# Kernel tuning notes

Measured on AMD Instinct MI355X. Metric: run time of the kernel, lower is better.

## Reference

```python
import jax, jax.numpy as jnp
import numpy as np
from jax.ops import segment_sum, segment_max

N = 50000   # nodes
E = 800000  # directed edges
H, C = 4, 64  # GAT heads, per-head channels (hidden_dim//4)
HID = 256
EPS = 1e-5


def setup_inputs() -> dict:
    key = jax.random.key(0)
    ks = jax.random.split(key, 24)
    g = lambda k, shape, fan: jax.random.normal(k, shape, jnp.float32) * (1.0 / np.sqrt(fan))
    inp = {
        'x': jax.random.normal(ks[0], (N, 3), jnp.float32),
        'edge_index': jax.random.randint(ks[1], (2, E), 0, N, jnp.int32),
        # GCNConv 1: 3 -> 64
        'W1': g(ks[2], (3, 64), 3), 'b1': jnp.zeros((64,), jnp.float32),
        # GCNConv 2: 64 -> 128
        'W2': g(ks[3], (64, 128), 64), 'b2': jnp.zeros((128,), jnp.float32),
        # GATConv: 128 -> 4 heads x 64
        'Wg': g(ks[4], (128, H * C), 128),
        'a_src': g(ks[5], (H, C), C), 'a_dst': g(ks[6], (H, C), C),
        'bg': jnp.zeros((H * C,), jnp.float32),
        # LayerNorms
        'ln1_g': jnp.ones((64,), jnp.float32), 'ln1_b': jnp.zeros((64,), jnp.float32),
        'ln2_g': jnp.ones((128,), jnp.float32), 'ln2_b': jnp.zeros((128,), jnp.float32),
        'ln3_g': jnp.ones((HID,), jnp.float32), 'ln3_b': jnp.zeros((HID,), jnp.float32),
        # GlobalAttention gate: Linear(256,256) ReLU Linear(256,1)
        'Wgt1': g(ks[7], (HID, HID), HID), 'bgt1': jnp.zeros((HID,), jnp.float32),
        'Wgt2': g(ks[8], (HID, 1), HID), 'bgt2': jnp.zeros((1,), jnp.float32),
        # output mlp: Linear(256,256) ReLU
        'Wm': g(ks[9], (HID, HID), HID), 'bm': jnp.zeros((HID,), jnp.float32),
    }
    return inp


def _ln(x, g, b):
    mu = x.mean(-1, keepdims=True)
    var = ((x - mu) ** 2).mean(-1, keepdims=True)
    return g * (x - mu) * jax.lax.rsqrt(var + EPS) + b


def reference(x, edge_index, W1, b1, W2, b2, Wg, a_src, a_dst, bg,
              ln1_g, ln1_b, ln2_g, ln2_b, ln3_g, ln3_b,
              Wgt1, bgt1, Wgt2, bgt2, Wm, bm):
    n = x.shape[0]
    loop = jnp.arange(n, dtype=edge_index.dtype)
    src = jnp.concatenate([edge_index[0], loop])  # self-loops added (PyG default)
    dst = jnp.concatenate([edge_index[1], loop])

    # symmetric GCN normalization (deg counts self-loop)
    deg = segment_sum(jnp.ones_like(src, jnp.float32), dst, num_segments=n)
    dinv = jax.lax.rsqrt(jnp.maximum(deg, 1.0))
    norm = (dinv[src] * dinv[dst])[:, None]  # [E+N,1]

    def gcn(h, W, b):
        h = h @ W
        return segment_sum(norm * h[src], dst, num_segments=n) + b

    x1 = _ln(jax.nn.relu(gcn(x, W1, b1)), ln1_g, ln1_b)
    x2 = _ln(jax.nn.relu(gcn(x1, W2, b2)), ln2_g, ln2_b)

    # GATConv: per-head scores, segment-softmax over destination
    h = (x2 @ Wg).reshape(n, H, C)
    s_src = (h * a_src).sum(-1)  # [N,H]
    s_dst = (h * a_dst).sum(-1)
    e = jax.nn.leaky_relu(s_src[src] + s_dst[dst], 0.2)  # [E+N,H]
    m = segment_max(e, dst, num_segments=n)
    ex = jnp.exp(e - m[dst])
    den = segment_sum(ex, dst, num_segments=n)
    alpha = ex / (den[dst] + 1e-16)  # [E+N,H]
    agg = segment_sum(alpha[:, :, None] * h[src], dst, num_segments=n)  # [N,H,C]
    x3 = _ln(agg.reshape(n, H * C) + bg, ln3_g, ln3_b)

    # GlobalAttention pooling (batch=None -> single graph)
    gate = jax.nn.relu(x3 @ Wgt1 + bgt1) @ Wgt2 + bgt2  # [N,1]
    w = jax.nn.softmax(gate, axis=0)
    pooled = (w * x3).sum(0, keepdims=True)  # [1,256]
    out = jax.nn.relu(pooled @ Wm + bm)  # [1,256]
    return out, x3
```

## Files before the change

### kernel.cpp

```cpp
#include <hip/hip_runtime.h>
#include <math.h>

#define NNODES 50000
#define NEDGES 800000

__device__ __forceinline__ float wave_sum(float v) {
#pragma unroll
  for (int o = 32; o > 0; o >>= 1) v += __shfl_xor(v, o, 64);
  return v;
}
__device__ __forceinline__ float wave_max(float v) {
#pragma unroll
  for (int o = 32; o > 0; o >>= 1) v = fmaxf(v, __shfl_xor(v, o, 64));
  return v;
}
template <int NW>
__device__ __forceinline__ float block_sum(float v, float* red) {
  v = wave_sum(v);
  __syncthreads();
  if ((threadIdx.x & 63) == 0) red[threadIdx.x >> 6] = v;
  __syncthreads();
  float s = 0.f;
#pragma unroll
  for (int i = 0; i < NW; i++) s += red[i];
  return s;
}

__device__ __forceinline__ float leaky02(float x) { return x > 0.f ? x : 0.2f * x; }

__device__ __forceinline__ void atomicMaxFloat(float* addr, float val) {
  if (val >= 0.f)
    atomicMax((int*)addr, __float_as_int(val));
  else
    atomicMin((unsigned int*)addr, __float_as_uint(val));
}

__global__ void k_init(int* __restrict__ deg, float* __restrict__ scal,
                       float* __restrict__ pooled) {
  int i = blockIdx.x * blockDim.x + threadIdx.x;
  if (i < NNODES) deg[i] = 0;
  if (i < 256) pooled[i] = 0.f;
  if (i == 0) { scal[0] = -3.0e38f; scal[1] = 0.f; }
}

__global__ void k_deg(const int* __restrict__ dst, int* __restrict__ deg) {
  int e = blockIdx.x * blockDim.x + threadIdx.x;
  if (e < NEDGES) atomicAdd(&deg[dst[e]], 1);
}

__global__ __launch_bounds__(1024) void k_scan(const int* __restrict__ deg,
                                               int* __restrict__ offs,
                                               int* __restrict__ cursor,
                                               float* __restrict__ dinv) {
  __shared__ int lds[1024];
  const int t = threadIdx.x;
  const int chunk = (NNODES + 1023) / 1024;
  int lo = t * chunk, hi = min(lo + chunk, NNODES);
  int s = 0;
  for (int i = lo; i < hi; i++) s += deg[i];
  lds[t] = s;
  __syncthreads();
  for (int off = 1; off < 1024; off <<= 1) {
    int v = (t >= off) ? lds[t - off] : 0;
    __syncthreads();
    lds[t] += v;
    __syncthreads();
  }
  int base = (t > 0) ? lds[t - 1] : 0;
  for (int i = lo; i < hi; i++) {
    int d = deg[i];
    offs[i] = base;
    cursor[i] = base;
    dinv[i] = rsqrtf((float)(d + 1));
    base += d;
  }
  if (t == 1023) offs[NNODES] = lds[1023];
}

__global__ void k_fill(const int* __restrict__ src, const int* __restrict__ dst,
                       int* __restrict__ cursor, int* __restrict__ csr) {
  int e = blockIdx.x * blockDim.x + threadIdx.x;
  if (e >= NEDGES) return;
  int d = dst[e];
  int p = atomicAdd(&cursor[d], 1);
  csr[p] = src[e];
}

__global__ void k_agg3(const float* __restrict__ x, const float* __restrict__ dinv,
                       const int* __restrict__ offs, const int* __restrict__ csr,
                       float* __restrict__ agg0) {
  int n = blockIdx.x * blockDim.x + threadIdx.x;
  if (n >= NNODES) return;
  float di = dinv[n];
  float a0 = di * x[n * 3], a1 = di * x[n * 3 + 1], a2 = di * x[n * 3 + 2];
  int lo = offs[n], hi = offs[n + 1];
  int p = lo;
  int snext = (p < hi) ? csr[p] : 0;
  while (p < hi) {
    int s = snext; p++; if (p < hi) snext = csr[p];
    float w = dinv[s];
    a0 = fmaf(w, x[s * 3], a0);
    a1 = fmaf(w, x[s * 3 + 1], a1);
    a2 = fmaf(w, x[s * 3 + 2], a2);
  }
  agg0[n * 3] = di * a0; agg0[n * 3 + 1] = di * a1; agg0[n * 3 + 2] = di * a2;
}

template <int VEC, int NG>
__global__ __launch_bounds__(64 * NG) void k_agg(const float* __restrict__ h,
                                                 const float* __restrict__ dinv,
                                                 const int* __restrict__ offs,
                                                 const int* __restrict__ csr,
                                                 float* __restrict__ out) {
  __shared__ float lacc[NG][64][VEC + 1];
  const int n = blockIdx.x;
  const int lane = threadIdx.x & 63, g = threadIdx.x >> 6;
  const float di = dinv[n];
  float acc[VEC];
#pragma unroll
  for (int v = 0; v < VEC; v++) acc[v] = 0.f;
  if (g == 0) {
    const float* r = h + (size_t)n * (64 * VEC) + lane * VEC;
#pragma unroll
    for (int v = 0; v < VEC; v++) acc[v] = di * r[v];
  }
  const int lo = offs[n], hi = offs[n + 1];
  int p = lo + g;
  int snext = (p < hi) ? csr[p] : 0;
  while (p < hi) {
    int s = snext; p += NG; if (p < hi) snext = csr[p];
    float w = dinv[s];
    const float* r = h + (size_t)s * (64 * VEC) + lane * VEC;
#pragma unroll
    for (int v = 0; v < VEC; v++) acc[v] = fmaf(w, r[v], acc[v]);
  }
#pragma unroll
  for (int v = 0; v < VEC; v++) lacc[g][lane][v] = acc[v];
  __syncthreads();
  if (g == 0) {
#pragma unroll
    for (int G = 1; G < NG; G++)
#pragma unroll
      for (int v = 0; v < VEC; v++) acc[v] += lacc[G][lane][v];
    float* o = out + (size_t)n * (64 * VEC) + lane * VEC;
#pragma unroll
    for (int v = 0; v < VEC; v++) o[v] = di * acc[v];
  }
}

template <int K, int M, int NT, bool RELU>
__global__ void k_mlp(const float* __restrict__ X, const float* __restrict__ W,
                      const float* __restrict__ b, const float* __restrict__ gam,
                      const float* __restrict__ bet, float* __restrict__ Y) {
  constexpr int NW = M / 64;
  __shared__ float xs[NT * K];
  __shared__ float red[NW];
  const int n0 = blockIdx.x * NT;
  const int j = threadIdx.x;
  const float4* Xt = (const float4*)(X + (size_t)n0 * K);
  for (int i = j; i < NT * K / 4; i += M) ((float4*)xs)[i] = Xt[i];
  __syncthreads();
  float acc[NT];
  float bj = b[j];
#pragma unroll
  for (int r = 0; r < NT; r++) acc[r] = bj;
  for (int k = 0; k < K; k++) {
    float wk = W[k * M + j];
#pragma unroll
    for (int r = 0; r < NT; r++) acc[r] = fmaf(xs[r * K + k], wk, acc[r]);
  }
  float gj = gam[j], btj = bet[j];
  for (int r = 0; r < NT; r++) {
    float a = RELU ? fmaxf(acc[r], 0.f) : acc[r];
    float mu = block_sum<NW>(a, red) * (1.f / M);
    float d = a - mu;
    float var = block_sum<NW>(d * d, red) * (1.f / M);
    Y[(size_t)(n0 + r) * M + j] = fmaf(gj * d, rsqrtf(var + 1e-5f), btj);
  }
}

__global__ void k_uvec(const float* __restrict__ Wg, const float* __restrict__ a_src,
                       const float* __restrict__ a_dst, float* __restrict__ u) {
  const int t = threadIdx.x;
  const int hh = t >> 7, k = t & 127;
  float us = 0.f, ud = 0.f;
  for (int c = 0; c < 64; c++) {
    float w = Wg[k * 256 + hh * 64 + c];
    us = fmaf(w, a_src[hh * 64 + c], us);
    ud = fmaf(w, a_dst[hh * 64 + c], ud);
  }
  u[t] = us;
  u[512 + t] = ud;
}

__global__ __launch_bounds__(256) void k_scores(const float* __restrict__ x2,
                                                const float* __restrict__ u,
                                                float* __restrict__ ssrc,
                                                float* __restrict__ sdst) {
  __shared__ float us[1024];
  const int t = threadIdx.x;
  for (int i = t; i < 1024; i += 256) us[i] = u[i];
  __syncthreads();
  const int n = blockIdx.x * 4 + (t >> 6);
  const int lane = t & 63;
  if (n >= NNODES) return;
  float2 xv = *(const float2*)(x2 + (size_t)n * 128 + lane * 2);
  float d[8];
#pragma unroll
  for (int h = 0; h < 4; h++) {
    d[h] = xv.x * us[h * 128 + lane * 2] + xv.y * us[h * 128 + lane * 2 + 1];
    d[4 + h] = xv.x * us[512 + h * 128 + lane * 2] + xv.y * us[512 + h * 128 + lane * 2 + 1];
  }
#pragma unroll
  for (int o = 32; o > 0; o >>= 1) {
#pragma unroll
    for (int i = 0; i < 8; i++) d[i] += __shfl_xor(d[i], o, 64);
  }
  if (lane == 0) {
    *(float4*)(ssrc + (size_t)n * 4) = make_float4(d[0], d[1], d[2], d[3]);
    *(float4*)(sdst + (size_t)n * 4) = make_float4(d[4], d[5], d[6], d[7]);
  }
}

__global__ __launch_bounds__(256) void k_gatagg(const float* __restrict__ x2,
                                                const float* __restrict__ ssrc,
                                                const float* __restrict__ sdst,
                                                const int* __restrict__ offs,
                                                const int* __restrict__ csr,
                                                float* __restrict__ aggx, int nbase) {
  __shared__ float lm[4][4];
  __shared__ float lden[4][4];
  __shared__ float lacc[4][64][9];
  const int n = nbase + blockIdx.x;
  const int t = threadIdx.x;
  const int lane = t & 63, g = t >> 6;
  const float4 sd = *(const float4*)(sdst + (size_t)n * 4);
  const int lo = offs[n], hi = offs[n + 1];
  float m0 = -3.4e38f, m1 = -3.4e38f, m2 = -3.4e38f, m3 = -3.4e38f;
  float e0x = 0.f, e0y = 0.f, e0z = 0.f, e0w = 0.f;
  if (g == 0) {
    float4 s0 = *(const float4*)(ssrc + (size_t)n * 4);
    e0x = leaky02(s0.x + sd.x); e0y = leaky02(s0.y + sd.y);
    e0z = leaky02(s0.z + sd.z); e0w = leaky02(s0.w + sd.w);
    m0 = e0x; m1 = e0y; m2 = e0z; m3 = e0w;
  }
  for (int p = lo + g; p < hi; p += 4) {
    int s = csr[p];
    float4 ss = *(const float4*)(ssrc + (size_t)s * 4);
    m0 = fmaxf(m0, leaky02(ss.x + sd.x));
    m1 = fmaxf(m1, leaky02(ss.y + sd.y));
    m2 = fmaxf(m2, leaky02(ss.z + sd.z));
    m3 = fmaxf(m3, leaky02(ss.w + sd.w));
  }
  if (lane == 0) { lm[g][0] = m0; lm[g][1] = m1; lm[g][2] = m2; lm[g][3] = m3; }
  __syncthreads();
  const float M0 = fmaxf(fmaxf(lm[0][0], lm[1][0]), fmaxf(lm[2][0], lm[3][0]));
  const float M1 = fmaxf(fmaxf(lm[0][1], lm[1][1]), fmaxf(lm[2][1], lm[3][1]));
  const float M2 = fmaxf(fmaxf(lm[0][2], lm[1][2]), fmaxf(lm[2][2], lm[3][2]));
  const float M3 = fmaxf(fmaxf(lm[0][3], lm[1][3]), fmaxf(lm[2][3], lm[3][3]));
  float den0 = 0.f, den1 = 0.f, den2 = 0.f, den3 = 0.f;
  float a0x = 0.f, a0y = 0.f, a1x = 0.f, a1y = 0.f;
  float a2x = 0.f, a2y = 0.f, a3x = 0.f, a3y = 0.f;
  if (g == 0) {
    float2 xv = *(const float2*)(x2 + (size_t)n * 128 + lane * 2);
    float w;
    w = __expf(e0x - M0); den0 = w; a0x = w * xv.x; a0y = w * xv.y;
    w = __expf(e0y - M1); den1 = w; a1x = w * xv.x; a1y = w * xv.y;
    w = __expf(e0z - M2); den2 = w; a2x = w * xv.x; a2y = w * xv.y;
    w = __expf(e0w - M3); den3 = w; a3x = w * xv.x; a3y = w * xv.y;
  }
  int p = lo + g;
  int snext = (p < hi) ? csr[p] : 0;
  while (p < hi) {
    int s = snext; p += 4; if (p < hi) snext = csr[p];
    float4 ss = *(const float4*)(ssrc + (size_t)s * 4);
    float2 xv = *(const float2*)(x2 + (size_t)s * 128 + lane * 2);
    float w0 = __expf(leaky02(ss.x + sd.x) - M0);
    float w1 = __expf(leaky02(ss.y + sd.y) - M1);
    float w2 = __expf(leaky02(ss.z + sd.z) - M2);
    float w3 = __expf(leaky02(ss.w + sd.w) - M3);
    den0 += w0; den1 += w1; den2 += w2; den3 += w3;
    a0x = fmaf(w0, xv.x, a0x); a0y = fmaf(w0, xv.y, a0y);
    a1x = fmaf(w1, xv.x, a1x); a1y = fmaf(w1, xv.y, a1y);
    a2x = fmaf(w2, xv.x, a2x); a2y = fmaf(w2, xv.y, a2y);
    a3x = fmaf(w3, xv.x, a3x); a3y = fmaf(w3, xv.y, a3y);
  }
  if (lane == 0) { lden[g][0] = den0; lden[g][1] = den1; lden[g][2] = den2; lden[g][3] = den3; }
  lacc[g][lane][0] = a0x; lacc[g][lane][1] = a0y;
  lacc[g][lane][2] = a1x; lacc[g][lane][3] = a1y;
  lacc[g][lane][4] = a2x; lacc[g][lane][5] = a2y;
  lacc[g][lane][6] = a3x; lacc[g][lane][7] = a3y;
  __syncthreads();
  float den = lden[0][g] + lden[1][g] + lden[2][g] + lden[3][g] + 1e-16f;
  float ax = lacc[0][lane][2 * g] + lacc[1][lane][2 * g] + lacc[2][lane][2 * g] + lacc[3][lane][2 * g];
  float ay = lacc[0][lane][2 * g + 1] + lacc[1][lane][2 * g + 1] + lacc[2][lane][2 * g + 1] + lacc[3][lane][2 * g + 1];
  float2 ov; ov.x = ax / den; ov.y = ay / den;
  *(float2*)(aggx + (size_t)blockIdx.x * 512 + g * 128 + lane * 2) = ov;
}

__global__ __launch_bounds__(256) void k_proj(const float* __restrict__ aggx,
                                              const float* __restrict__ Wg,
                                              const float* __restrict__ bg,
                                              const float* __restrict__ gam,
                                              const float* __restrict__ bet,
                                              float* __restrict__ x3, int nbase) {
  __shared__ float xs[8 * 512];
  __shared__ float red[4];
  const int r0 = blockIdx.x * 8;
  const int j = threadIdx.x;
  const int head = j >> 6;
  const float4* At = (const float4*)(aggx + (size_t)r0 * 512);
  for (int i = j; i < 1024; i += 256) ((float4*)xs)[i] = At[i];
  __syncthreads();
  float acc[8];
  float bgj = bg[j];
#pragma unroll
  for (int r = 0; r < 8; r++) acc[r] = bgj;
  for (int k = 0; k < 128; k++) {
    float wk = Wg[k * 256 + j];
#pragma unroll
    for (int r = 0; r < 8; r++) acc[r] = fmaf(xs[r * 512 + head * 128 + k], wk, acc[r]);
  }
  float gj = gam[j], btj = bet[j];
  for (int r = 0; r < 8; r++) {
    float a = acc[r];
    float mu = block_sum<4>(a, red) * (1.f / 256.f);
    float d = a - mu;
    float var = block_sum<4>(d * d, red) * (1.f / 256.f);
    x3[(size_t)(nbase + r0 + r) * 256 + j] = fmaf(gj * d, rsqrtf(var + 1e-5f), btj);
  }
}

__global__ __launch_bounds__(256) void k_gate(const float* __restrict__ x3,
                                              const float* __restrict__ Wgt1,
                                              const float* __restrict__ bgt1,
                                              const float* __restrict__ Wgt2,
                                              const float* __restrict__ bgt2,
                                              float* __restrict__ gate) {
  __shared__ float xs[16 * 256];
  __shared__ float hs[16 * 256];
  const int n0 = blockIdx.x * 16;
  const int j = threadIdx.x;
  const float4* Xt = (const float4*)(x3 + (size_t)n0 * 256);
  for (int i = j; i < 1024; i += 256) ((float4*)xs)[i] = Xt[i];
  __syncthreads();
  float acc[16];
  float b1j = bgt1[j];
#pragma unroll
  for (int r = 0; r < 16; r++) acc[r] = b1j;
  for (int k = 0; k < 256; k++) {
    float wk = Wgt1[k * 256 + j];
#pragma unroll
    for (int r = 0; r < 16; r++) acc[r] = fmaf(xs[r * 256 + k], wk, acc[r]);
  }
  float w2 = Wgt2[j];
#pragma unroll
  for (int r = 0; r < 16; r++) hs[r * 256 + j] = fmaxf(acc[r], 0.f) * w2;
  __syncthreads();
  const int wv = j >> 6, lane = j & 63;
  float b2 = bgt2[0];
#pragma unroll
  for (int rr = 0; rr < 4; rr++) {
    int r = wv * 4 + rr;
    float s = hs[r * 256 + lane] + hs[r * 256 + 64 + lane] +
              hs[r * 256 + 128 + lane] + hs[r * 256 + 192 + lane];
    s = wave_sum(s);
    if (lane == 0) gate[n0 + r] = s + b2;
  }
}

__global__ void k_gmax(const float* __restrict__ gate, float* __restrict__ scal) {
  __shared__ float red[4];
  int i = blockIdx.x * 256 + threadIdx.x;
  float v = (i < NNODES) ? gate[i] : -3.0e38f;
  v = wave_max(v);
  __syncthreads();
  if ((threadIdx.x & 63) == 0) red[threadIdx.x >> 6] = v;
  __syncthreads();
  if (threadIdx.x == 0) {
    float m = fmaxf(fmaxf(red[0], red[1]), fmaxf(red[2], red[3]));
    atomicMaxFloat(&scal[0], m);
  }
}

__global__ void k_pool(const float* __restrict__ x3, const float* __restrict__ gate,
                       const float* __restrict__ scal, float* __restrict__ pooled) {
  const int c = threadIdx.x;
  const float gmax = scal[0];
  float acc = 0.f, zl = 0.f;
  for (int node = blockIdx.x; node < NNODES; node += gridDim.x) {
    float wv = __expf(gate[node] - gmax);
    if (c == 0) zl += wv;
    acc = fmaf(wv, x3[(size_t)node * 256 + c], acc);
  }
  atomicAdd(&pooled[c], acc);
  if (c == 0) atomicAdd((float*)&scal[1], zl);
}

__global__ void k_out(const float* __restrict__ pooled, const float* __restrict__ scal,
                      const float* __restrict__ Wm, const float* __restrict__ bm,
                      float* __restrict__ out) {
  __shared__ float p[256];
  const int j = threadIdx.x;
  p[j] = pooled[j] / scal[1];
  __syncthreads();
  float acc = bm[j];
  for (int k = 0; k < 256; k++) acc = fmaf(p[k], Wm[k * 256 + j], acc);
  out[j] = fmaxf(acc, 0.f);
}

extern "C" void kernel_launch(void* const* d_in, const int* in_sizes, int n_in,
                              void* d_out, int out_size, void* d_ws, size_t ws_size,
                              hipStream_t stream) {
  const float* x     = (const float*)d_in[0];
  const int*   ei    = (const int*)d_in[1];
  const float* W1    = (const float*)d_in[2];
  const float* b1    = (const float*)d_in[3];
  const float* W2    = (const float*)d_in[4];
  const float* b2    = (const float*)d_in[5];
  const float* Wg    = (const float*)d_in[6];
  const float* a_src = (const float*)d_in[7];
  const float* a_dst = (const float*)d_in[8];
  const float* bg    = (const float*)d_in[9];
  const float* ln1g  = (const float*)d_in[10];
  const float* ln1b  = (const float*)d_in[11];
  const float* ln2g  = (const float*)d_in[12];
  const float* ln2b  = (const float*)d_in[13];
  const float* ln3g  = (const float*)d_in[14];
  const float* ln3b  = (const float*)d_in[15];
  const float* Wgt1  = (const float*)d_in[16];
  const float* bgt1  = (const float*)d_in[17];
  const float* Wgt2  = (const float*)d_in[18];
  const float* bgt2  = (const float*)d_in[19];
  const float* Wm    = (const float*)d_in[20];
  const float* bm    = (const float*)d_in[21];

  float* out = (float*)d_out;
  float* x3  = out + 256;

  const int* src = ei;
  const int* dst = ei + NEDGES;

  char* wsb = (char*)d_ws;
  size_t off = 0;
  auto carve = [&](size_t bytes) -> void* {
    void* p = wsb + off;
    off += (bytes + 255) & ~(size_t)255;
    return p;
  };
  int*   deg    = (int*)carve((size_t)NNODES * 4);
  int*   offs   = (int*)carve((size_t)(NNODES + 1) * 4);
  int*   cursor = (int*)carve((size_t)NNODES * 4);
  int*   csr    = (int*)carve((size_t)NEDGES * 4);
  float* dinv   = (float*)carve((size_t)NNODES * 4);
  float* bufA   = (float*)carve((size_t)NNODES * 256 * 4);
  float* x2     = (float*)carve((size_t)NNODES * 128 * 4);
  float* ssrc   = (float*)carve((size_t)NNODES * 4 * 4);
  float* sdst   = (float*)carve((size_t)NNODES * 4 * 4);
  float* u      = (float*)carve(1024 * 4);
  float* gate   = (float*)carve((size_t)NNODES * 4);
  float* pooled = (float*)carve(256 * 4);
  float* scal   = (float*)carve(2 * 4);

  float* x1   = bufA;
  float* agg1 = bufA + (size_t)NNODES * 64;
  float* agg0 = bufA + (size_t)NNODES * 128;
  float* aggx = bufA;

  k_init<<<(NNODES + 255) / 256, 256, 0, stream>>>(deg, scal, pooled);
  k_deg<<<NEDGES / 256, 256, 0, stream>>>(dst, deg);
  k_scan<<<1, 1024, 0, stream>>>(deg, offs, cursor, dinv);
  k_fill<<<NEDGES / 256, 256, 0, stream>>>(src, dst, cursor, csr);

  k_agg3<<<(NNODES + 255) / 256, 256, 0, stream>>>(x, dinv, offs, csr, agg0);
  k_mlp<3, 64, 16, true><<<NNODES / 16, 64, 0, stream>>>(agg0, W1, b1, ln1g, ln1b, x1);

  k_agg<1, 4><<<NNODES, 256, 0, stream>>>(x1, dinv, offs, csr, agg1);
  k_mlp<64, 128, 8, true><<<NNODES / 8, 128, 0, stream>>>(agg1, W2, b2, ln2g, ln2b, x2);

  k_uvec<<<1, 512, 0, stream>>>(Wg, a_src, a_dst, u);
  k_scores<<<(NNODES + 3) / 4, 256, 0, stream>>>(x2, u, ssrc, sdst);
  for (int c = 0; c < 2; c++) {
    int nbase = c * (NNODES / 2);
    k_gatagg<<<NNODES / 2, 256, 0, stream>>>(x2, ssrc, sdst, offs, csr, aggx, nbase);
    k_proj<<<NNODES / 2 / 8, 256, 0, stream>>>(aggx, Wg, bg, ln3g, ln3b, x3, nbase);
  }

  k_gate<<<NNODES / 16, 256, 0, stream>>>(x3, Wgt1, bgt1, Wgt2, bgt2, gate);
  k_gmax<<<(NNODES + 255) / 256, 256, 0, stream>>>(gate, scal);
  k_pool<<<256, 256, 0, stream>>>(x3, gate, scal, pooled);
  k_out<<<1, 256, 0, stream>>>(pooled, scal, Wm, bm, out);
}
```

Before: 957.2 us.

## Register-tile the GAT projection and gate GEMMs with 4x4 per-thread outputs

Rewrites k_proj and k_gate so each thread computes a 4-row by 4-column output tile using float4 loads of both the shared-memory activations and the global weights. Each weight and activation value loaded is then reused across four outputs instead of one. LayerNorm and the gate reduction become per-wave shuffles, which removes the block-wide __syncthreads reductions and the hs shared buffer. k_proj now handles 16 rows per block, pads its shared rows to stride 132, and adds bounds checks. The cost is more registers per thread and fewer blocks in flight for k_proj.

```diff
diff --git a/kernel.cpp b/kernel.cpp
--- a/kernel.cpp
+++ b/kernel.cpp
@@ -303,31 +303,73 @@
                                               const float* __restrict__ bg,
                                               const float* __restrict__ gam,
                                               const float* __restrict__ bet,
-                                              float* __restrict__ x3, int nbase) {
-  __shared__ float xs[8 * 512];
-  __shared__ float red[4];
-  const int r0 = blockIdx.x * 8;
-  const int j = threadIdx.x;
-  const int head = j >> 6;
-  const float4* At = (const float4*)(aggx + (size_t)r0 * 512);
-  for (int i = j; i < 1024; i += 256) ((float4*)xs)[i] = At[i];
-  __syncthreads();
-  float acc[8];
-  float bgj = bg[j];
-#pragma unroll
-  for (int r = 0; r < 8; r++) acc[r] = bgj;
-  for (int k = 0; k < 128; k++) {
-    float wk = Wg[k * 256 + j];
-#pragma unroll
-    for (int r = 0; r < 8; r++) acc[r] = fmaf(xs[r * 512 + head * 128 + k], wk, acc[r]);
-  }
-  float gj = gam[j], btj = bet[j];
-  for (int r = 0; r < 8; r++) {
-    float a = acc[r];
-    float mu = block_sum<4>(a, red) * (1.f / 256.f);
-    float d = a - mu;
-    float var = block_sum<4>(d * d, red) * (1.f / 256.f);
-    x3[(size_t)(nbase + r0 + r) * 256 + j] = fmaf(gj * d, rsqrtf(var + 1e-5f), btj);
+                                              float* __restrict__ x3, int nbase,
+                                              int nrows) {
+  __shared__ float xs[16][4 * 132];
+  const int r0 = blockIdx.x * 16;
+  const int t = threadIdx.x;
+  const int cq = t & 63, rq = t >> 6;
+  const int h = cq >> 4;
+  for (int idx = t; idx < 16 * 128; idx += 256) {
+    int r = idx >> 7;
+    int p = (idx & 127) << 2;
+    int hh = p >> 7, k = p & 127;
+    float4 v = (r0 + r < nrows)
+                   ? *(const float4*)(aggx + (size_t)(r0 + r) * 512 + p)
+                   : make_float4(0.f, 0.f, 0.f, 0.f);
+    *(float4*)&xs[r][hh * 132 + k] = v;
+  }
+  __syncthreads();
+  float acc[4][4];
+#pragma unroll
+  for (int i = 0; i < 4; i++)
+#pragma unroll
+    for (int j = 0; j < 4; j++) acc[i][j] = 0.f;
+  const float4* Wv = (const float4*)Wg;
+  for (int k0 = 0; k0 < 128; k0 += 4) {
+    float4 xk[4], wk[4];
+#pragma unroll
+    for (int i = 0; i < 4; i++)
+      xk[i] = *(const float4*)&xs[rq * 4 + i][h * 132 + k0];
+#pragma unroll
+    for (int kk = 0; kk < 4; kk++) wk[kk] = Wv[(size_t)(k0 + kk) * 64 + cq];
+#pragma unroll
+    for (int kk = 0; kk < 4; kk++) {
+      const float* wf = (const float*)&wk[kk];
+#pragma unroll
+      for (int i = 0; i < 4; i++) {
+        const float* xf = (const float*)&xk[i];
+        float xv = xf[kk];
+#pragma unroll
+        for (int j = 0; j < 4; j++) acc[i][j] = fmaf(xv, wf[j], acc[i][j]);
+      }
+    }
+  }
+  float4 bgv = *(const float4*)(bg + cq * 4);
+  float4 gav = *(const float4*)(gam + cq * 4);
+  float4 bev = *(const float4*)(bet + cq * 4);
+  const float* bgf = (const float*)&bgv;
+  const float* gaf = (const float*)&gav;
+  const float* bef = (const float*)&bev;
+#pragma unroll
+  for (int i = 0; i < 4; i++) {
+    float a[4], s = 0.f;
+#pragma unroll
+    for (int j = 0; j < 4; j++) { a[j] = acc[i][j] + bgf[j]; s += a[j]; }
+    float mu = wave_sum(s) * (1.f / 256.f);
+    float s2 = 0.f;
+#pragma unroll
+    for (int j = 0; j < 4; j++) { float d = a[j] - mu; s2 += d * d; }
+    float rs = rsqrtf(wave_sum(s2) * (1.f / 256.f) + 1e-5f);
+    int r = r0 + rq * 4 + i;
+    if (r < nrows) {
+      float4 ov;
+      ov.x = fmaf(gaf[0] * (a[0] - mu), rs, bef[0]);
+      ov.y = fmaf(gaf[1] * (a[1] - mu), rs, bef[1]);
+      ov.z = fmaf(gaf[2] * (a[2] - mu), rs, bef[2]);
+      ov.w = fmaf(gaf[3] * (a[3] - mu), rs, bef[3]);
+      *(float4*)(x3 + (size_t)(nbase + r) * 256 + cq * 4) = ov;
+    }
   }
 }
 
@@ -337,35 +379,52 @@
                                               const float* __restrict__ Wgt2,
                                               const float* __restrict__ bgt2,
                                               float* __restrict__ gate) {
-  __shared__ float xs[16 * 256];
-  __shared__ float hs[16 * 256];
+  __shared__ float xs[16][256];
   const int n0 = blockIdx.x * 16;
-  const int j = threadIdx.x;
-  const float4* Xt = (const float4*)(x3 + (size_t)n0 * 256);
-  for (int i = j; i < 1024; i += 256) ((float4*)xs)[i] = Xt[i];
-  __syncthreads();
-  float acc[16];
-  float b1j = bgt1[j];
-#pragma unroll
-  for (int r = 0; r < 16; r++) acc[r] = b1j;
-  for (int k = 0; k < 256; k++) {
-    float wk = Wgt1[k * 256 + j];
-#pragma unroll
-    for (int r = 0; r < 16; r++) acc[r] = fmaf(xs[r * 256 + k], wk, acc[r]);
-  }
-  float w2 = Wgt2[j];
-#pragma unroll
-  for (int r = 0; r < 16; r++) hs[r * 256 + j] = fmaxf(acc[r], 0.f) * w2;
-  __syncthreads();
-  const int wv = j >> 6, lane = j & 63;
+  const int t = threadIdx.x;
+  const int cq = t & 63, rq = t >> 6;
+  for (int idx = t; idx < 16 * 64; idx += 256) {
+    int r = idx >> 6, p = (idx & 63) << 2;
+    *(float4*)&xs[r][p] = *(const float4*)(x3 + (size_t)(n0 + r) * 256 + p);
+  }
+  __syncthreads();
+  float acc[4][4];
+#pragma unroll
+  for (int i = 0; i < 4; i++)
+#pragma unroll
+    for (int j = 0; j < 4; j++) acc[i][j] = 0.f;
+  const float4* Wv = (const float4*)Wgt1;
+  for (int k0 = 0; k0 < 256; k0 += 4) {
+    float4 xk[4], wk[4];
+#pragma unroll
+    for (int i = 0; i < 4; i++) xk[i] = *(const float4*)&xs[rq * 4 + i][k0];
+#pragma unroll
+    for (int kk = 0; kk < 4; kk++) wk[kk] = Wv[(size_t)(k0 + kk) * 64 + cq];
+#pragma unroll
+    for (int kk = 0; kk < 4; kk++) {
+      const float* wf = (const float*)&wk[kk];
+#pragma unroll
+      for (int i = 0; i < 4; i++) {
+        const float* xf = (const float*)&xk[i];
+        float xv = xf[kk];
+#pragma unroll
+        for (int j = 0; j < 4; j++) acc[i][j] = fmaf(xv, wf[j], acc[i][j]);
+      }
+    }
+  }
+  float4 b1v = *(const float4*)(bgt1 + cq * 4);
+  float4 w2v = *(const float4*)(Wgt2 + cq * 4);
+  const float* b1f = (const float*)&b1v;
+  const float* w2f = (const float*)&w2v;
   float b2 = bgt2[0];
 #pragma unroll
-  for (int rr = 0; rr < 4; rr++) {
-    int r = wv * 4 + rr;
-    float s = hs[r * 256 + lane] + hs[r * 256 + 64 + lane] +
-              hs[r * 256 + 128 + lane] + hs[r * 256 + 192 + lane];
+  for (int i = 0; i < 4; i++) {
+    float s = 0.f;
+#pragma unroll
+    for (int j = 0; j < 4; j++)
+      s = fmaf(fmaxf(acc[i][j] + b1f[j], 0.f), w2f[j], s);
     s = wave_sum(s);
-    if (lane == 0) gate[n0 + r] = s + b2;
+    if (cq == 0) gate[n0 + rq * 4 + i] = s + b2;
   }
 }
 
@@ -482,8 +541,10 @@
   k_scores<<<(NNODES + 3) / 4, 256, 0, stream>>>(x2, u, ssrc, sdst);
   for (int c = 0; c < 2; c++) {
     int nbase = c * (NNODES / 2);
-    k_gatagg<<<NNODES / 2, 256, 0, stream>>>(x2, ssrc, sdst, offs, csr, aggx, nbase);
-    k_proj<<<NNODES / 2 / 8, 256, 0, stream>>>(aggx, Wg, bg, ln3g, ln3b, x3, nbase);
+    int nrows = NNODES / 2;
+    k_gatagg<<<nrows, 256, 0, stream>>>(x2, ssrc, sdst, offs, csr, aggx, nbase);
+    k_proj<<<(nrows + 15) / 16, 256, 0, stream>>>(aggx, Wg, bg, ln3g, ln3b, x3,
+                                                  nbase, nrows);
   }
 
   k_gate<<<NNODES / 16, 256, 0, stream>>>(x3, Wgt1, bgt1, Wgt2, bgt2, gate);
```

New measurement: 922.5 us. 1.04x faster.
